# Performance work log

Measured on AMD Instinct MI355X. Metric: run time of the kernel, lower is better.

The kernel has to match this reference:

```python
import jax, jax.numpy as jnp
import numpy as np

WINDOW_SIZE = 11
SIGMA = 1.5
C1 = 0.01 ** 2
C2 = 0.03 ** 2
L1_WEIGHT = 1.0
SSIM_WEIGHT = 1.0


def _gaussian_window(channels, window_size=WINDOW_SIZE, sigma=SIGMA):
    x = np.arange(window_size, dtype=np.float32) - window_size // 2
    g = np.exp(-(x ** 2) / (2.0 * sigma ** 2))
    g = g / g.sum()
    w2d = np.outer(g, g).astype(np.float32)  # [ws, ws]
    # depthwise kernel layout OIHW with I=1, O=channels
    return jnp.asarray(np.tile(w2d[None, None], (channels, 1, 1, 1)))


def _dwconv(x, w):
    pad = WINDOW_SIZE // 2
    return jax.lax.conv_general_dilated(
        x, w, window_strides=(1, 1), padding=[(pad, pad), (pad, pad)],
        dimension_numbers=('NCHW', 'OIHW', 'NCHW'),
        feature_group_count=x.shape[1])


def setup_inputs() -> dict:
    key = jax.random.key(0)
    k1, k2 = jax.random.split(key)
    shape = (16, 3, 512, 512)
    outputs = jax.random.uniform(k1, shape, dtype=jnp.float32)
    labels = jax.random.uniform(k2, shape, dtype=jnp.float32)
    return {"outputs": outputs, "labels": labels}


def reference(outputs, labels):
    img1, img2 = outputs, labels
    channel = img1.shape[1]
    window = _gaussian_window(channel).astype(img1.dtype)

    mu1 = _dwconv(img1, window)
    mu2 = _dwconv(img2, window)
    mu1_sq = mu1 * mu1
    mu2_sq = mu2 * mu2
    mu1_mu2 = mu1 * mu2
    sigma1_sq = _dwconv(img1 * img1, window) - mu1_sq
    sigma2_sq = _dwconv(img2 * img2, window) - mu2_sq
    sigma12 = _dwconv(img1 * img2, window) - mu1_mu2

    ssim_map = ((2 * mu1_mu2 + C1) * (2 * sigma12 + C2)) / (
        (mu1_sq + mu2_sq + C1) * (sigma1_sq + sigma2_sq + C2))
    ssim = jnp.mean(ssim_map)

    l1_loss = jnp.mean(jnp.abs(outputs - labels))
    ssim_loss = 1.0 - ssim
    return L1_WEIGHT * l1_loss + SSIM_WEIGHT * ssim_loss
```

## Files before the change

kernel.cpp:

```cpp
#include <hip/hip_runtime.h>
#include <hip/hip_bf16.h>
#include <math.h>

#define IMG 512
#define TW 64
#define TH 32
#define NTX 8
#define NTY 16
#define NIMG 48
#define NBLOCKS (NTX * NTY * NIMG)
#define NPIX (16LL * 3 * 512 * 512)

#define C1F 0.0001f
#define C2F 0.0009f

#define SROWS 42
#define SR 88

typedef __attribute__((ext_vector_type(4))) short short4v;
typedef __attribute__((ext_vector_type(8))) short short8;
typedef __attribute__((ext_vector_type(4))) float float4v;
typedef __attribute__((ext_vector_type(2))) unsigned uint2v;
typedef __attribute__((ext_vector_type(4))) unsigned uint4v;

__device__ __forceinline__ float4v mfma16(short4v a, short4v b, float4v c) {
#if defined(__HIP_DEVICE_COMPILE__)
    return __builtin_amdgcn_mfma_f32_16x16x16bf16_1k(a, b, c, 0, 0, 0);
#else
    return c;
#endif
}

#define GW0 0.00102838f
#define GW1 0.00759877f
#define GW2 0.03600077f
#define GW3 0.10936069f
#define GW4 0.21300539f
#define GW5 0.26601172f

__device__ __forceinline__ unsigned short f2bf(float f) {
    unsigned u = __builtin_bit_cast(unsigned, f);
    u += 0x7FFF + ((u >> 16) & 1);
    return (unsigned short)(u >> 16);
}
__device__ __forceinline__ unsigned pk2(float a, float b) {
    __hip_bfloat162 h = __float22bfloat162_rn(make_float2(a, b));
    unsigned u;
    __builtin_memcpy(&u, &h, 4);
    return u;
}

__global__ __launch_bounds__(256, 5)
void ssim_tile_kernel(const float* __restrict__ xg, const float* __restrict__ yg,
                      float* __restrict__ partials) {
    __shared__ unsigned short sbuf[4][SROWS][SR];
    __shared__ unsigned short gwtbl[16];
    __shared__ float red[8];

    const int tid  = threadIdx.x;
    const int lane = tid & 63;
    const int w    = tid >> 6;
    const int q    = lane >> 4;
    const int n16  = lane & 15;

    const int img = blockIdx.z;
    const int r00  = blockIdx.y * TH - 5;
    const int c00a = blockIdx.x * TW - 8;
    const float* __restrict__ xi = xg + (size_t)img * (IMG * IMG);
    const float* __restrict__ yi = yg + (size_t)img * (IMG * IMG);

    if (tid < 16) {
        const float gwf[11] = {GW0, GW1, GW2, GW3, GW4, GW5, GW4, GW3, GW2, GW1, GW0};
        unsigned short v = 0;
        #pragma unroll
        for (int t = 0; t < 11; ++t)
            if (tid == t) v = f2bf(gwf[t]);
        gwtbl[tid] = v;
    }

    float l1_loc = 0.f;
    #pragma unroll
    for (int it = 0; it < 2; ++it) {
        int u = tid + it * 256;
        if (it == 0 || tid < 420 - 256) {
            int pr  = u / 10;
            int g10 = u - pr * 10;
            int pc8 = g10 << 3;
            int gr = r00 + pr, gc = c00a + pc8;
            float4 x0 = make_float4(0.f, 0.f, 0.f, 0.f), x1 = x0;
            float4 y0 = x0, y1 = x0;
            bool rowok = (unsigned)gr < 512u;
            size_t o = (size_t)gr * IMG + gc;
            if (rowok && (unsigned)gc < 512u) {
                x0 = *(const float4*)(xi + o);
                y0 = *(const float4*)(yi + o);
            }
            if (rowok && (unsigned)(gc + 4) < 512u) {
                x1 = *(const float4*)(xi + o + 4);
                y1 = *(const float4*)(yi + o + 4);
            }
            *(uint4v*)&sbuf[0][pr][pc8] = (uint4v){
                pk2(x0.x, x0.y), pk2(x0.z, x0.w), pk2(x1.x, x1.y), pk2(x1.z, x1.w)};
            *(uint4v*)&sbuf[1][pr][pc8] = (uint4v){
                pk2(y0.x, y0.y), pk2(y0.z, y0.w), pk2(y1.x, y1.y), pk2(y1.z, y1.w)};
            *(uint4v*)&sbuf[2][pr][pc8] = (uint4v){
                pk2(fmaf(x0.x, x0.x, y0.x * y0.x), fmaf(x0.y, x0.y, y0.y * y0.y)),
                pk2(fmaf(x0.z, x0.z, y0.z * y0.z), fmaf(x0.w, x0.w, y0.w * y0.w)),
                pk2(fmaf(x1.x, x1.x, y1.x * y1.x), fmaf(x1.y, x1.y, y1.y * y1.y)),
                pk2(fmaf(x1.z, x1.z, y1.z * y1.z), fmaf(x1.w, x1.w, y1.w * y1.w))};
            *(uint4v*)&sbuf[3][pr][pc8] = (uint4v){
                pk2(x0.x * y0.x, x0.y * y0.y), pk2(x0.z * y0.z, x0.w * y0.w),
                pk2(x1.x * y1.x, x1.y * y1.y), pk2(x1.z * y1.z, x1.w * y1.w)};
            if ((unsigned)(pr - 5) <= 31u && (unsigned)(g10 - 1) <= 7u)
                l1_loc += fabsf(x0.x - y0.x) + fabsf(x0.y - y0.y)
                        + fabsf(x0.z - y0.z) + fabsf(x0.w - y0.w)
                        + fabsf(x1.x - y1.x) + fabsf(x1.y - y1.y)
                        + fabsf(x1.z - y1.z) + fabsf(x1.w - y1.w);
        }
    }
    __syncthreads();

    short8 bh;
    short4v bv0, bv1;
    {
        int baseh = q * 8 - n16 - 3;
        #pragma unroll
        for (int j = 0; j < 8; ++j)
            bh[j] = (short)gwtbl[min((unsigned)(baseh + j), 15u)];
        int base0 = q * 4 - n16, base1 = q * 4 + 16 - n16;
        #pragma unroll
        for (int j = 0; j < 4; ++j) {
            bv0[j] = (short)gwtbl[min((unsigned)(base0 + j), 15u)];
            bv1[j] = (short)gwtbl[min((unsigned)(base1 + j), 15u)];
        }
    }

    const float4v zero4 = {0.f, 0.f, 0.f, 0.f};
    uint2v d1[3][4];
    #pragma unroll
    for (int rg = 0; rg < 3; ++rg) {
        int row = rg * 16 + n16;
        if (rg == 2) row = min(row, 41);
        const int co = w * 16 + q * 8;
        #pragma unroll
        for (int ch = 0; ch < 4; ++ch) {
            short8 a = *(const short8*)&sbuf[ch][row][co];
            float4v d = __builtin_amdgcn_mfma_f32_16x16x32_bf16(a, bh, zero4, 0, 0, 0);
            d1[rg][ch] = (uint2v){pk2(d[0], d[1]), pk2(d[2], d[3])};
        }
    }

    float ssim_loc = 0.f;
    #pragma unroll
    for (int rgp = 0; rgp < 2; ++rgp) {
        float4v acc4[4];
        #pragma unroll
        for (int ch = 0; ch < 4; ++ch) {
            short4v a1 = __builtin_bit_cast(short4v, d1[rgp + 1][ch]);
            short4v a0 = __builtin_bit_cast(short4v, d1[rgp][ch]);
            acc4[ch] = mfma16(a0, bv0, mfma16(a1, bv1, zero4));
        }
        #pragma unroll
        for (int r = 0; r < 4; ++r) {
            float mu1 = acc4[0][r], mu2 = acc4[1][r];
            float e   = acc4[2][r], e12 = acc4[3][r];
            float p = mu1 * mu2;
            float s = fmaf(mu1, mu1, mu2 * mu2);
            float num1 = fmaf(2.f, p, C1F);
            float num2 = fmaf(2.f, e12 - p, C2F);
            float den1 = s + C1F;
            float den2 = (e - s) + C2F;
            ssim_loc = fmaf(num1 * num2, __builtin_amdgcn_rcpf(den1 * den2), ssim_loc);
        }
    }

    #pragma unroll
    for (int off = 32; off > 0; off >>= 1) {
        ssim_loc += __shfl_down(ssim_loc, off);
        l1_loc   += __shfl_down(l1_loc, off);
    }
    if (lane == 0) {
        red[w] = ssim_loc;
        red[4 + w] = l1_loc;
    }
    __syncthreads();
    if (tid == 0) {
        float ss = red[0] + red[1] + red[2] + red[3];
        float ll = red[4] + red[5] + red[6] + red[7];
        int bid = blockIdx.x + NTX * (blockIdx.y + NTY * blockIdx.z);
        partials[bid] = ss;
        partials[NBLOCKS + bid] = ll;
    }
}

__global__ __launch_bounds__(1024)
void finalize_kernel(const float* __restrict__ partials, float* __restrict__ out) {
    __shared__ double rs[16], rl[16];
    const int tid = threadIdx.x;
    double ss = 0.0, ll = 0.0;
    for (int i = tid; i < NBLOCKS; i += 1024) {
        ss += (double)partials[i];
        ll += (double)partials[NBLOCKS + i];
    }
    #pragma unroll
    for (int off = 32; off > 0; off >>= 1) {
        ss += __shfl_down(ss, off);
        ll += __shfl_down(ll, off);
    }
    int wave = tid >> 6, lane = tid & 63;
    if (lane == 0) { rs[wave] = ss; rl[wave] = ll; }
    __syncthreads();
    if (tid == 0) {
        double sst = 0.0, llt = 0.0;
        #pragma unroll
        for (int w = 0; w < 16; ++w) { sst += rs[w]; llt += rl[w]; }
        double invn = 1.0 / (double)NPIX;
        out[0] = (float)(llt * invn + (1.0 - sst * invn));
    }
}

extern "C" void kernel_launch(void* const* d_in, const int* in_sizes, int n_in,
                              void* d_out, int out_size, void* d_ws, size_t ws_size,
                              hipStream_t stream) {
    const float* x = (const float*)d_in[0];
    const float* y = (const float*)d_in[1];
    float* out = (float*)d_out;
    float* partials = (float*)d_ws;

    dim3 grid(NTX, NTY, NIMG);
    ssim_tile_kernel<<<grid, dim3(256), 0, stream>>>(x, y, partials);
    finalize_kernel<<<1, dim3(1024), 0, stream>>>(partials, out);
}
```

Baseline: 131.9 us.

## Compute squared and product channels from bf16 LDS tiles instead of storing them

Shared memory now holds only the x and y tiles in bf16, which halves LDS use. The x²+y² and x·y channels are recomputed in registers from the bf16 values just before the horizontal MFMA pass, and the launch-bound occupancy hint rises from 5 to 8 blocks. The aim is more resident blocks and fewer LDS writes, at the cost of extra ALU work and a change in precision: the products are now formed from bf16-rounded inputs rather than fp32 inputs.

```diff
diff --git a/kernel.cpp b/kernel.cpp
--- a/kernel.cpp
+++ b/kernel.cpp
@@ -49,11 +49,14 @@
     __builtin_memcpy(&u, &h, 4);
     return u;
 }
-
-__global__ __launch_bounds__(256, 5)
+__device__ __forceinline__ float bf2f(short s) {
+    return __builtin_bit_cast(float, (unsigned)(unsigned short)s << 16);
+}
+
+__global__ __launch_bounds__(256, 8)
 void ssim_tile_kernel(const float* __restrict__ xg, const float* __restrict__ yg,
                       float* __restrict__ partials) {
-    __shared__ unsigned short sbuf[4][SROWS][SR];
+    __shared__ unsigned short sbuf[2][SROWS][SR];
     __shared__ unsigned short gwtbl[16];
     __shared__ float red[8];
 
@@ -103,14 +106,6 @@
                 pk2(x0.x, x0.y), pk2(x0.z, x0.w), pk2(x1.x, x1.y), pk2(x1.z, x1.w)};
             *(uint4v*)&sbuf[1][pr][pc8] = (uint4v){
                 pk2(y0.x, y0.y), pk2(y0.z, y0.w), pk2(y1.x, y1.y), pk2(y1.z, y1.w)};
-            *(uint4v*)&sbuf[2][pr][pc8] = (uint4v){
-                pk2(fmaf(x0.x, x0.x, y0.x * y0.x), fmaf(x0.y, x0.y, y0.y * y0.y)),
-                pk2(fmaf(x0.z, x0.z, y0.z * y0.z), fmaf(x0.w, x0.w, y0.w * y0.w)),
-                pk2(fmaf(x1.x, x1.x, y1.x * y1.x), fmaf(x1.y, x1.y, y1.y * y1.y)),
-                pk2(fmaf(x1.z, x1.z, y1.z * y1.z), fmaf(x1.w, x1.w, y1.w * y1.w))};
-            *(uint4v*)&sbuf[3][pr][pc8] = (uint4v){
-                pk2(x0.x * y0.x, x0.y * y0.y), pk2(x0.z * y0.z, x0.w * y0.w),
-                pk2(x1.x * y1.x, x1.y * y1.y), pk2(x1.z * y1.z, x1.w * y1.w)};
             if ((unsigned)(pr - 5) <= 31u && (unsigned)(g10 - 1) <= 7u)
                 l1_loc += fabsf(x0.x - y0.x) + fabsf(x0.y - y0.y)
                         + fabsf(x0.z - y0.z) + fabsf(x0.w - y0.w)
@@ -142,12 +137,27 @@
         int row = rg * 16 + n16;
         if (rg == 2) row = min(row, 41);
         const int co = w * 16 + q * 8;
-        #pragma unroll
-        for (int ch = 0; ch < 4; ++ch) {
-            short8 a = *(const short8*)&sbuf[ch][row][co];
-            float4v d = __builtin_amdgcn_mfma_f32_16x16x32_bf16(a, bh, zero4, 0, 0, 0);
-            d1[rg][ch] = (uint2v){pk2(d[0], d[1]), pk2(d[2], d[3])};
-        }
+        short8 ax = *(const short8*)&sbuf[0][row][co];
+        short8 ay = *(const short8*)&sbuf[1][row][co];
+        uint4v u2, u3;
+        #pragma unroll
+        for (int jj = 0; jj < 4; ++jj) {
+            float xa = bf2f(ax[2 * jj]),     ya = bf2f(ay[2 * jj]);
+            float xb = bf2f(ax[2 * jj + 1]), yb = bf2f(ay[2 * jj + 1]);
+            u2[jj] = pk2(fmaf(xa, xa, ya * ya), fmaf(xb, xb, yb * yb));
+            u3[jj] = pk2(xa * ya, xb * yb);
+        }
+        float4v d;
+        d = __builtin_amdgcn_mfma_f32_16x16x32_bf16(ax, bh, zero4, 0, 0, 0);
+        d1[rg][0] = (uint2v){pk2(d[0], d[1]), pk2(d[2], d[3])};
+        d = __builtin_amdgcn_mfma_f32_16x16x32_bf16(ay, bh, zero4, 0, 0, 0);
+        d1[rg][1] = (uint2v){pk2(d[0], d[1]), pk2(d[2], d[3])};
+        d = __builtin_amdgcn_mfma_f32_16x16x32_bf16(
+                __builtin_bit_cast(short8, u2), bh, zero4, 0, 0, 0);
+        d1[rg][2] = (uint2v){pk2(d[0], d[1]), pk2(d[2], d[3])};
+        d = __builtin_amdgcn_mfma_f32_16x16x32_bf16(
+                __builtin_bit_cast(short8, u3), bh, zero4, 0, 0, 0);
+        d1[rg][3] = (uint2v){pk2(d[0], d[1]), pk2(d[2], d[3])};
     }
 
     float ssim_loc = 0.f;
```

Measured after the change: 136.7 us. 3.7% more time.
